# Kernel optimization log

Hardware: AMD Instinct MI355X
Metric: run time of the kernel (lower is better)

Reference implementation:

```python
import jax, jax.numpy as jnp
import numpy as np
import math

B, S, E, H, L = 16, 512, 256, 4, 2
D = E // H            # head size = 64
MAX_POS = 10
NUM_ITEMS = 50000


def setup_inputs() -> dict:
    key = jax.random.key(0)
    ks = jax.random.split(key, 16)
    s = 0.02
    item_inputs = jax.random.randint(ks[0], (B, S), 0, 2 * NUM_ITEMS + 1)
    item_ids = jax.random.randint(ks[1], (B, S), 0, NUM_ITEMS)
    input_embed = jax.random.normal(ks[2], (2 * NUM_ITEMS + 1, E), jnp.float32) * s
    input_embed = input_embed.at[0].set(0.0)  # padding_idx=0
    query_embed = jax.random.normal(ks[3], (NUM_ITEMS, E), jnp.float32) * s
    pos_key = jax.random.normal(ks[4], (MAX_POS, D), jnp.float32) * s
    pos_value = jax.random.normal(ks[5], (MAX_POS, D), jnp.float32) * s
    Wq = jax.random.normal(ks[6], (L, E, E), jnp.float32) * s
    bq = jnp.zeros((L, E), jnp.float32)
    Wk = jax.random.normal(ks[7], (L, E, E), jnp.float32) * s
    bk = jnp.zeros((L, E), jnp.float32)
    Wv = jax.random.normal(ks[8], (L, E, E), jnp.float32) * s
    bv = jnp.zeros((L, E), jnp.float32)
    Wo = jax.random.normal(ks[9], (L, E, E), jnp.float32) * s
    bo = jnp.zeros((L, E), jnp.float32)
    out_w = jax.random.normal(ks[10], (E, 1), jnp.float32) * s
    out_b = jnp.zeros((1,), jnp.float32)
    return dict(item_inputs=item_inputs, item_ids=item_ids,
                input_embed=input_embed, query_embed=query_embed,
                pos_key=pos_key, pos_value=pos_value,
                Wq=Wq, bq=bq, Wk=Wk, bk=bk, Wv=Wv, bv=bv, Wo=Wo, bo=bo,
                out_w=out_w, out_b=out_b)


def _heads(x, W, b):
    # [B,S,E] @ [E,E] -> [B,H,S,D]
    return (x @ W + b).reshape(B, S, H, D).transpose(0, 2, 1, 3)


def reference(item_inputs, item_ids, input_embed, query_embed, pos_key,
              pos_value, Wq, bq, Wk, bk, Wv, bv, Wo, bo, out_w, out_b):
    x = input_embed[item_inputs]          # [B,S,E]
    q_base = query_embed[item_ids]        # [B,S,E]

    i = jnp.arange(S)
    rel = jnp.clip(i[:, None] - i[None, :], 0, MAX_POS - 1)  # [S,S]
    pk = pos_key[rel]                     # [S,S,D]
    pv = pos_value[rel]                   # [S,S,D]
    causal = i[None, :] > i[:, None]      # future mask [S,S], True = masked
    scale = 1.0 / math.sqrt(D)

    out = x
    for l in range(L):
        qh = _heads(q_base, Wq[l], bq[l])
        kh = _heads(out, Wk[l], bk[l])
        vh = _heads(out, Wv[l], bv[l])
        # relative attention: scores = q.k^T + q.pos_key(i-j)
        scores = jnp.einsum('bhid,bhjd->bhij', qh, kh)
        scores = scores + jnp.einsum('bhid,ijd->bhij', qh, pk)
        scores = scores * scale
        scores = jnp.where(causal[None, None], -1e9, scores)
        p = jax.nn.softmax(scores, axis=-1)  # [B,H,S,S]
        # out_i = sum_j p_ij * (v_j + pos_value(i-j))
        attn = jnp.einsum('bhij,bhjd->bhid', p, vh) \
             + jnp.einsum('bhij,ijd->bhid', p, pv)
        merged = attn.transpose(0, 2, 1, 3).reshape(B, S, E)
        residual = merged @ Wo[l] + bo[l]
        out = out + jax.nn.relu(residual)
    return out @ out_w + out_b            # [B,S,1]
```

## Files before the change

### kernel.cpp

```cpp
#include <hip/hip_runtime.h>
#include <hip/hip_bf16.h>

#define B_ 16
#define S_ 512
#define E_ 256
#define H_ 4
#define D_ 64
#define L_ 2
#define MAXPOS 10
#define HS_ ((size_t)B_ * S_ * E_)

typedef __attribute__((ext_vector_type(8))) short bf16x8;
typedef __attribute__((ext_vector_type(4))) float f32x4;

static __device__ __forceinline__ short f2bf(float f) {
    __hip_bfloat16 h = __float2bfloat16(f);
    return __builtin_bit_cast(short, h);
}

static __device__ __forceinline__ void gload16(const void* g, void* l) {
    __builtin_amdgcn_global_load_lds(
        (const __attribute__((address_space(1))) void*)(g),
        (__attribute__((address_space(3))) void*)(l),
        16, 0, 0);
}

static __device__ __forceinline__ void stage_tile(const char* gbase, char* lds,
                                                  int w, int lane) {
    #pragma unroll
    for (int c = 0; c < 8; ++c) {
        const int L = (w * 8 + c) * 1024 + lane * 16;
        const int src = L ^ (((L >> 9) & 7) << 4);
        gload16(gbase + src, lds + (w * 8 + c) * 1024);
    }
}

static __device__ __forceinline__ void gemm4(const short* As, const short* Bs,
                                             int w, int l15, int l4,
                                             f32x4& a0, f32x4& a1,
                                             f32x4& a2, f32x4& a3) {
    const int sw = (l15 & 7) << 4;
    const int arow = w * 16 + l15;
    const f32x4 z4 = (f32x4){0.f, 0.f, 0.f, 0.f};
    a0 = z4; a1 = z4; a2 = z4; a3 = z4;
    #pragma unroll
    for (int ks = 0; ks < 8; ++ks) {
        const int coff = (ks * 64 + l4 * 16) ^ sw;
        const bf16x8 af = *reinterpret_cast<const bf16x8*>((const char*)As + arow * 512 + coff);
        const bf16x8 b0 = *reinterpret_cast<const bf16x8*>((const char*)Bs + (0 * 16 + l15) * 512 + coff);
        a0 = __builtin_amdgcn_mfma_f32_16x16x32_bf16(af, b0, a0, 0, 0, 0);
        const bf16x8 b1 = *reinterpret_cast<const bf16x8*>((const char*)Bs + (1 * 16 + l15) * 512 + coff);
        a1 = __builtin_amdgcn_mfma_f32_16x16x32_bf16(af, b1, a1, 0, 0, 0);
        const bf16x8 b2 = *reinterpret_cast<const bf16x8*>((const char*)Bs + (2 * 16 + l15) * 512 + coff);
        a2 = __builtin_amdgcn_mfma_f32_16x16x32_bf16(af, b2, a2, 0, 0, 0);
        const bf16x8 b3 = *reinterpret_cast<const bf16x8*>((const char*)Bs + (3 * 16 + l15) * 512 + coff);
        a3 = __builtin_amdgcn_mfma_f32_16x16x32_bf16(af, b3, a3, 0, 0, 0);
    }
}

static __device__ __forceinline__ void gemm_compute(const short* As, const short* Bs,
                                                    f32x4* acc, int w, int l15, int l4) {
    gemm4(As, Bs, w, l15, l4, acc[0], acc[1], acc[2], acc[3]);
}

__global__ __launch_bounds__(256) void setup_kernel(
    const int* __restrict__ item_inputs, const int* __restrict__ item_ids,
    const float* __restrict__ input_embed, const float* __restrict__ query_embed,
    const float* __restrict__ Wq, const float* __restrict__ Wk,
    const float* __restrict__ Wv, const float* __restrict__ Wo,
    const float* __restrict__ out_b,
    short* __restrict__ outb, short* __restrict__ qbb,
    short* __restrict__ Wt, float* __restrict__ y)
{
    const int tid = threadIdx.x;
    const int bx = blockIdx.x;
    if (bx < 512) {
        const int rr = tid >> 4, c0 = (tid & 15) * 16;
        const int row = bx * 16 + rr;
        const int ii = item_inputs[row];
        const int qi = item_ids[row];
        const float* xs = input_embed + (size_t)ii * E_ + c0;
        const float* qs = query_embed + (size_t)qi * E_ + c0;
        short* ob = outb + (size_t)row * E_ + c0;
        short* qb = qbb + (size_t)row * E_ + c0;
        #pragma unroll
        for (int q = 0; q < 4; ++q) {
            const float4 xv = reinterpret_cast<const float4*>(xs)[q];
            const float4 qv = reinterpret_cast<const float4*>(qs)[q];
            short4 xb = { f2bf(xv.x), f2bf(xv.y), f2bf(xv.z), f2bf(xv.w) };
            short4 qb4 = { f2bf(qv.x), f2bf(qv.y), f2bf(qv.z), f2bf(qv.w) };
            reinterpret_cast<short4*>(ob)[q] = xb;
            reinterpret_cast<short4*>(qb)[q] = qb4;
        }
        return;
    }
    const int pb = bx - 512;
    if (pb < 128) {
        __shared__ short tt[64 * 72];
        const int mId = pb >> 4;
        const int l = mId >> 2, which = mId & 3;
        const float* src = (which == 0 ? Wq : which == 1 ? Wk : which == 2 ? Wv : Wo)
                         + (size_t)l * E_ * E_;
        const int tr = (pb >> 2) & 3;
        const int tc = pb & 3;
        {
            const int kl = tid >> 2;
            const int nq = (tid & 3) * 16;
            const float* sp = src + (size_t)(tr * 64 + kl) * E_ + tc * 64 + nq;
            #pragma unroll
            for (int q = 0; q < 4; ++q) {
                const float4 v = reinterpret_cast<const float4*>(sp)[q];
                tt[(nq + q * 4 + 0) * 72 + kl] = f2bf(v.x);
                tt[(nq + q * 4 + 1) * 72 + kl] = f2bf(v.y);
                tt[(nq + q * 4 + 2) * 72 + kl] = f2bf(v.z);
                tt[(nq + q * 4 + 3) * 72 + kl] = f2bf(v.w);
            }
        }
        __syncthreads();
        {
            const int nl = tid >> 2;
            const int kq = (tid & 3) * 16;
            short* dst = Wt + (size_t)mId * 65536 + (size_t)(tc * 64 + nl) * E_ + tr * 64 + kq;
            *reinterpret_cast<bf16x8*>(&dst[0]) = *reinterpret_cast<const bf16x8*>(&tt[nl * 72 + kq]);
            *reinterpret_cast<bf16x8*>(&dst[8]) = *reinterpret_cast<const bf16x8*>(&tt[nl * 72 + kq + 8]);
        }
    } else if (pb == 128) {
        const float yb = out_b[0];
        for (int i = tid; i < 8192; i += 256) y[i] = yb;
    }
}

__global__ __launch_bounds__(256) void qkv0_kernel(
    const short* __restrict__ qbb, const short* __restrict__ outb,
    const short* __restrict__ Wt, const float* __restrict__ bq,
    const float* __restrict__ bk, const float* __restrict__ bv,
    const float* __restrict__ bq1, short* __restrict__ Qb,
    short* __restrict__ Qb1)
{
    __shared__ __align__(16) short As[64 * 256];
    __shared__ __align__(16) short Bs[64 * 256];
    const int bid = blockIdx.x;
    const int logical = (bid & 7) * 192 + (bid >> 3);
    const int bm = logical / 12;
    const int r = logical % 12;
    const int bn = r / 3, zp = r % 3;
    const int tid = threadIdx.x;
    const int lane = tid & 63, w = tid >> 6;
    const int l15 = lane & 15, l4 = lane >> 4;

    const short* A = (zp == 0) ? qbb : outb;
    const short* W0 = Wt + (size_t)zp * 65536;
    const float* bias0 = (zp == 0) ? bq : (zp == 1) ? bk : bv;
    short* C0 = Qb + (size_t)zp * HS_;

    stage_tile((const char*)A + (size_t)bm * 32768, (char*)As, w, lane);
    stage_tile((const char*)W0 + (size_t)bn * 32768, (char*)Bs, w, lane);
    __syncthreads();

    f32x4 acc[4];
    gemm_compute(As, Bs, acc, w, l15, l4);

    #pragma unroll
    for (int nf = 0; nf < 4; ++nf) {
        const int col = bn * 64 + nf * 16 + l15;
        const float bb = bias0[col];
        #pragma unroll
        for (int reg = 0; reg < 4; ++reg) {
            const int rowg = bm * 64 + w * 16 + l4 * 4 + reg;
            C0[(size_t)rowg * E_ + col] = f2bf(acc[nf][reg] + bb);
        }
    }

    if (zp == 0) {
        __syncthreads();
        stage_tile((const char*)(Wt + (size_t)4 * 65536) + (size_t)bn * 32768,
                   (char*)Bs, w, lane);
        __syncthreads();
        gemm_compute(As, Bs, acc, w, l15, l4);
        #pragma unroll
        for (int nf = 0; nf < 4; ++nf) {
            const int col = bn * 64 + nf * 16 + l15;
            const float bb = bq1[col];
            #pragma unroll
            for (int reg = 0; reg < 4; ++reg) {
                const int rowg = bm * 64 + w * 16 + l4 * 4 + reg;
                Qb1[(size_t)rowg * E_ + col] = f2bf(acc[nf][reg] + bb);
            }
        }
    }
}

__global__ __launch_bounds__(256) void kv1_kernel(
    const short* __restrict__ outb, const short* __restrict__ Wt1,
    const float* __restrict__ bk1, const float* __restrict__ bv1,
    short* __restrict__ Qb)
{
    __shared__ __align__(16) short As[64 * 256];
    __shared__ __align__(16) short Bs[64 * 256];
    const int bid = blockIdx.x;
    const int logical = (bid & 7) * 128 + (bid >> 3);
    const int bm = logical >> 3;
    const int r = logical & 7;
    const int bn = r >> 1, z = r & 1;
    const int tid = threadIdx.x;
    const int lane = tid & 63, w = tid >> 6;
    const int l15 = lane & 15, l4 = lane >> 4;

    const short* W = Wt1 + (size_t)(z + 1) * 65536;
    const float* bias = (z == 0) ? bk1 : bv1;

    stage_tile((const char*)outb + (size_t)bm * 32768, (char*)As, w, lane);
    stage_tile((const char*)W + (size_t)bn * 32768, (char*)Bs, w, lane);
    __syncthreads();

    f32x4 acc[4];
    gemm_compute(As, Bs, acc, w, l15, l4);

    short* Cz = Qb + (size_t)(z + 1) * HS_;
    #pragma unroll
    for (int nf = 0; nf < 4; ++nf) {
        const int col = bn * 64 + nf * 16 + l15;
        const float bb = bias[col];
        #pragma unroll
        for (int reg = 0; reg < 4; ++reg) {
            const int rowg = bm * 64 + w * 16 + l4 * 4 + reg;
            Cz[(size_t)rowg * E_ + col] = f2bf(acc[nf][reg] + bb);
        }
    }
}

__global__ __launch_bounds__(256) void o0_kernel(
    const short* __restrict__ mgb, const short* __restrict__ Wo_t,
    const float* __restrict__ bo0, const int* __restrict__ item_inputs,
    const float* __restrict__ input_embed, float* __restrict__ outf,
    short* __restrict__ outb)
{
    __shared__ __align__(16) short As[64 * 256];
    __shared__ __align__(16) short Bs[64 * 256];
    const int bid = blockIdx.x;
    const int logical = (bid & 7) * 64 + (bid >> 3);
    const int bm = logical >> 2, bn = logical & 3;
    const int tid = threadIdx.x;
    const int lane = tid & 63, w = tid >> 6;
    const int l15 = lane & 15, l4 = lane >> 4;

    stage_tile((const char*)mgb + (size_t)bm * 32768, (char*)As, w, lane);
    stage_tile((const char*)Wo_t + (size_t)bn * 32768, (char*)Bs, w, lane);
    __syncthreads();

    f32x4 acc[4];
    gemm_compute(As, Bs, acc, w, l15, l4);

    #pragma unroll
    for (int reg = 0; reg < 4; ++reg) {
        const int rowg = bm * 64 + w * 16 + l4 * 4 + reg;
        const int ii = item_inputs[rowg];
        const float* emb = input_embed + (size_t)ii * E_;
        #pragma unroll
        for (int nf = 0; nf < 4; ++nf) {
            const int col = bn * 64 + nf * 16 + l15;
            const size_t idx = (size_t)rowg * E_ + col;
            const float o = emb[col] + fmaxf(acc[nf][reg] + bo0[col], 0.0f);
            outf[idx] = o;
            outb[idx] = f2bf(o);
        }
    }
}

__global__ __launch_bounds__(256) void attn_kernel(
    const short* __restrict__ Q, const short* __restrict__ K,
    const short* __restrict__ V, const float* __restrict__ pos_key,
    const float* __restrict__ pos_value, short* __restrict__ merged)
{
    __shared__ __align__(16) short Qs[64 * 72];
    __shared__ __align__(16) short Ks[2][64 * 64];
    __shared__ __align__(16) short Vts[2][4656];
    __shared__ __align__(16) short Pl[4 * 16 * 72];
    __shared__ __align__(16) short Pk[16 * 72];
    __shared__ float pv_sh[MAXPOS * 64];
    __shared__ float qpk_sh[64 * 16];
    __shared__ float pdiag[64 * 9];

    const int bid = blockIdx.x;
    const int half = bid >> 8;
    const int g = bid & 255;
    const int tp = g & 3;
    const int bh = g >> 2;
    const int it = half ? tp : 7 - tp;
    const int h = bh & 3;
    const int b = bh >> 2;
    const int tid = threadIdx.x;
    const int lane = tid & 63;
    const int w = tid >> 6;
    const int l15 = lane & 15;
    const int l4  = lane >> 4;
    const int rloc  = l4 * 4;
    const int rbase = w * 16 + rloc;
    const int swl = (l15 & 7) << 4;
    const float SC = 0.18033688f;

    const size_t boff = (size_t)(b * S_) * E_ + h * D_;

    const int vrow = tid >> 2, vdq = (tid & 3) * 16;
    const int vskew = (tid & 3) * 32 + vrow * 2;
    auto issueK = [&](int jt, int buf) {
        const char* Kb = (const char*)(K + boff + (size_t)(jt * 64) * E_);
        #pragma unroll
        for (int c = 0; c < 2; ++c) {
            const int chunk = w * 2 + c;
            const int row = chunk * 8 + (lane >> 3);
            const int col = (lane & 7) * 16;
            const int src = row * 512 + (col ^ ((row & 7) << 4));
            gload16(Kb + src, (char*)Ks[buf] + chunk * 1024);
        }
    };
    auto issueV = [&](int jt, bf16x8& v0, bf16x8& v1) {
        const short* vp = &V[boff + (size_t)(jt * 64 + vrow) * E_ + vdq];
        v0 = *reinterpret_cast<const bf16x8*>(vp);
        v1 = *reinterpret_cast<const bf16x8*>(vp + 8);
    };
    auto writeV = [&](int buf, const bf16x8& v0, const bf16x8& v1) {
        #pragma unroll
        for (int e = 0; e < 8; ++e) {
            *(short*)((char*)Vts[buf] + (vdq + e) * 144 + vskew) = v0[e];
            *(short*)((char*)Vts[buf] + (vdq + 8 + e) * 144 + vskew) = v1[e];
        }
    };

    issueK(0, 0);
    bf16x8 vc0, vc1;
    issueV(0, vc0, vc1);

    for (int idx = tid; idx < MAXPOS * 64; idx += 256) pv_sh[idx] = pos_value[idx];
    for (int idx = tid; idx < 64 * 9; idx += 256) pdiag[idx] = 0.0f;
    for (int idx = tid; idx < 16 * 64; idx += 256) {
        const int r = idx >> 6, d = idx & 63;
        Pk[r * 72 + d] = (r < MAXPOS) ? f2bf(pos_key[r * 64 + d]) : (short)0;
    }
    {
        const int row = tid >> 2, dq = (tid & 3) * 16;
        const short* qp = &Q[boff + (size_t)(it * 64 + row) * E_ + dq];
        *reinterpret_cast<bf16x8*>(&Qs[row * 72 + dq]) = *reinterpret_cast<const bf16x8*>(qp);
        *reinterpret_cast<bf16x8*>(&Qs[row * 72 + dq + 8]) = *reinterpret_cast<const bf16x8*>(qp + 8);
    }
    writeV(0, vc0, vc1);
    __syncthreads();

    bf16x8 aq[2];
    #pragma unroll
    for (int ks = 0; ks < 2; ++ks)
        aq[ks] = *reinterpret_cast<const bf16x8*>(&Qs[(w * 16 + l15) * 72 + ks * 32 + 8 * l4]);

    f32x4 cq = (f32x4){0.f, 0.f, 0.f, 0.f};
    #pragma unroll
    for (int ks = 0; ks < 2; ++ks) {
        const bf16x8 bpk = *reinterpret_cast<const bf16x8*>(&Pk[l15 * 72 + ks * 32 + 8 * l4]);
        cq = __builtin_amdgcn_mfma_f32_16x16x32_bf16(aq[ks], bpk, cq, 0, 0, 0);
    }
    float q9[4];
    #pragma unroll
    for (int r = 0; r < 4; ++r) {
        qpk_sh[(rbase + r) * 16 + l15] = cq[r] * SC;
        q9[r] = __shfl(cq[r], l4 * 16 + 9, 64) * SC;
    }

    f32x4 accv[4];
    #pragma unroll
    for (int nf = 0; nf < 4; ++nf) accv[nf] = (f32x4){0.f, 0.f, 0.f, 0.f};
    float ls[4] = {0.f, 0.f, 0.f, 0.f};

    for (int jt = 0; jt <= it; ++jt) {
        const int cur = jt & 1;
        bf16x8 vn0, vn1;
        if (jt < it) {
            issueK(jt + 1, cur ^ 1);
            issueV(jt + 1, vn0, vn1);
        }

        f32x4 cs[4];
        __builtin_amdgcn_s_setprio(1);
        #pragma unroll
        for (int nf = 0; nf < 4; ++nf) {
            const int jrow = nf * 16 + l15;
            const bf16x8 bk0 = *reinterpret_cast<const bf16x8*>(
                (const char*)Ks[cur] + jrow * 128 + ((l4 * 16) ^ swl));
            const bf16x8 bk1 = *reinterpret_cast<const bf16x8*>(
                (const char*)Ks[cur] + jrow * 128 + ((64 + l4 * 16) ^ swl));
            f32x4 c = (f32x4){0.f, 0.f, 0.f, 0.f};
            c = __builtin_amdgcn_mfma_f32_16x16x32_bf16(aq[0], bk0, c, 0, 0, 0);
            cs[nf] = __builtin_amdgcn_mfma_f32_16x16x32_bf16(aq[1], bk1, c, 0, 0, 0);
        }
        __builtin_amdgcn_s_setprio(0);

        const bool near = (jt >= it - 1);
        #pragma unroll
        for (int nf = 0; nf < 4; ++nf) {
            const int j = jt * 64 + nf * 16 + l15;
            #pragma unroll
            for (int r = 0; r < 4; ++r) {
                float pp;
                if (near) {
                    const int i = it * 64 + rbase + r;
                    const int rel = i - j;
                    if (rel < 0) pp = 0.0f;
                    else {
                        const int rc = rel < 9 ? rel : 9;
                        pp = exp2f(fmaf(cs[nf][r], SC, qpk_sh[(rbase + r) * 16 + rc]));
                        if (rel < 9) pdiag[(rbase + r) * 9 + rel] = pp;
                    }
                } else {
                    pp = exp2f(fmaf(cs[nf][r], SC, q9[r]));
                }
                ls[r] += pp;
                Pl[w * 1152 + (rloc + r) * 72 + nf * 16 + l15] = f2bf(pp);
            }
        }

        __builtin_amdgcn_s_setprio(1);
        #pragma unroll
        for (int ks = 0; ks < 2; ++ks) {
            const bf16x8 pa = *reinterpret_cast<const bf16x8*>(
                &Pl[w * 1152 + l15 * 72 + ks * 32 + 8 * l4]);
            #pragma unroll
            for (int nf = 0; nf < 4; ++nf) {
                const int d = nf * 16 + l15;
                const bf16x8 bv = *reinterpret_cast<const bf16x8*>(
                    (const char*)Vts[cur] + d * 144 + nf * 32 + ks * 64 + l4 * 16);
                accv[nf] = __builtin_amdgcn_mfma_f32_16x16x32_bf16(pa, bv, accv[nf], 0, 0, 0);
            }
        }
        __builtin_amdgcn_s_setprio(0);

        if (jt < it) {
            writeV(cur ^ 1, vn0, vn1);
            __syncthreads();
        }
    }

    #pragma unroll
    for (int m = 1; m < 16; m <<= 1) {
        #pragma unroll
        for (int r = 0; r < 4; ++r) ls[r] += __shfl_xor(ls[r], m, 64);
    }

    #pragma unroll
    for (int r = 0; r < 4; ++r) {
        const int rowl = rbase + r;
        const float inv = 1.0f / ls[r];
        #pragma unroll
        for (int nf = 0; nf < 4; ++nf) {
            const int col = nf * 16 + l15;
            const float pv9 = pv_sh[9 * 64 + col];
            float extra = ls[r] * pv9;
            #pragma unroll
            for (int rr = 0; rr < 9; ++rr)
                extra += pdiag[rowl * 9 + rr] * (pv_sh[rr * 64 + col] - pv9);
            merged[boff + (size_t)(it * 64 + rowl) * E_ + col] =
                f2bf((accv[nf][r] + extra) * inv);
        }
    }
}

__global__ __launch_bounds__(256) void o1final_kernel(
    const short* __restrict__ mgb, const short* __restrict__ Wt7,
    const float* __restrict__ bo1, const float* __restrict__ outf,
    const float* __restrict__ fw, float* __restrict__ y)
{
    __shared__ __align__(16) short As[64 * 256];
    __shared__ __align__(16) short Bs[64 * 256];
    const int bid = blockIdx.x;
    const int logical = (bid & 7) * 64 + (bid >> 3);
    const int bm = logical >> 2, bn = logical & 3;
    const int tid = threadIdx.x;
    const int lane = tid & 63, w = tid >> 6;
    const int l15 = lane & 15, l4 = lane >> 4;

    stage_tile((const char*)mgb + (size_t)bm * 32768, (char*)As, w, lane);
    stage_tile((const char*)Wt7 + (size_t)bn * 32768, (char*)Bs, w, lane);
    __syncthreads();

    f32x4 acc[4];
    gemm_compute(As, Bs, acc, w, l15, l4);

    float s[4] = {0.f, 0.f, 0.f, 0.f};
    #pragma unroll
    for (int nf = 0; nf < 4; ++nf) {
        const int col = bn * 64 + nf * 16 + l15;
        const float bb = bo1[col];
        const float fwv = fw[col];
        #pragma unroll
        for (int reg = 0; reg < 4; ++reg) {
            const int rowg = bm * 64 + w * 16 + l4 * 4 + reg;
            const float o = outf[(size_t)rowg * E_ + col] + fmaxf(acc[nf][reg] + bb, 0.0f);
            s[reg] += o * fwv;
        }
    }
    #pragma unroll
    for (int m = 1; m < 16; m <<= 1) {
        #pragma unroll
        for (int reg = 0; reg < 4; ++reg) s[reg] += __shfl_xor(s[reg], m, 64);
    }
    if (l15 == 0) {
        #pragma unroll
        for (int reg = 0; reg < 4; ++reg)
            atomicAdd(&y[bm * 64 + w * 16 + l4 * 4 + reg], s[reg]);
    }
}

extern "C" void kernel_launch(void* const* d_in, const int* in_sizes, int n_in,
                              void* d_out, int out_size, void* d_ws, size_t ws_size,
                              hipStream_t stream) {
    const int*   item_inputs = (const int*)d_in[0];
    const int*   item_ids    = (const int*)d_in[1];
    const float* input_embed = (const float*)d_in[2];
    const float* query_embed = (const float*)d_in[3];
    const float* pos_key     = (const float*)d_in[4];
    const float* pos_value   = (const float*)d_in[5];
    const float* Wq = (const float*)d_in[6];
    const float* bq = (const float*)d_in[7];
    const float* Wk = (const float*)d_in[8];
    const float* bk = (const float*)d_in[9];
    const float* Wv = (const float*)d_in[10];
    const float* bv = (const float*)d_in[11];
    const float* Wo = (const float*)d_in[12];
    const float* bo = (const float*)d_in[13];
    const float* out_w = (const float*)d_in[14];
    const float* out_b = (const float*)d_in[15];
    float* y = (float*)d_out;

    char* w8 = (char*)d_ws;
    float* outf = (float*)(w8);
    short* outb = (short*)(w8 + ((size_t)8  << 20));
    short* qbb  = (short*)(w8 + ((size_t)12 << 20));
    short* Qb   = (short*)(w8 + ((size_t)16 << 20));
    short* mgb  = (short*)(w8 + ((size_t)28 << 20));
    short* Wt   = (short*)(w8 + ((size_t)32 << 20));
    short* Qb1  = (short*)(w8 + ((size_t)34 << 20));

    setup_kernel<<<641, 256, 0, stream>>>(
        item_inputs, item_ids, input_embed, query_embed,
        Wq, Wk, Wv, Wo, out_b, outb, qbb, Wt, y);

    qkv0_kernel<<<1536, 256, 0, stream>>>(
        qbb, outb, Wt, bq, bk, bv, bq + E_, Qb, Qb1);
    attn_kernel<<<512, 256, 0, stream>>>(
        Qb, Qb + HS_, Qb + 2 * HS_, pos_key, pos_value, mgb);
    o0_kernel<<<512, 256, 0, stream>>>(
        mgb, Wt + (size_t)3 * 65536, bo, item_inputs, input_embed, outf, outb);

    kv1_kernel<<<1024, 256, 0, stream>>>(
        outb, Wt + (size_t)4 * 65536, bk + E_, bv + E_, Qb);
    attn_kernel<<<512, 256, 0, stream>>>(
        Qb1, Qb + HS_, Qb + 2 * HS_, pos_key, pos_value, mgb);
    o1final_kernel<<<512, 256, 0, stream>>>(
        mgb, Wt + (size_t)7 * 65536, bo + E_, outf, out_w, y);
}
```

Baseline: 91.76 us.

## Fuse embedding gather and weight transpose into the layer-0 QKV GEMM kernel

Removes the separate setup kernel. The layer-0 QKV GEMM blocks now gather embedding rows, convert them to bf16 and write them straight into swizzled LDS. They also read the fp32 Wq/Wk/Wv directly, transposing them into LDS instead of staging pre-converted bf16 tiles. Extra blocks in the same launch transpose only the weights later kernels need (Wo0, Wk1, Wv1, Wo1) and initialise y. This saves a launch and the bf16 intermediate round trip. In exchange, every GEMM block redundantly converts fp32 weights and embeddings, using scalar 2-byte LDS stores, which may be costly.

```diff
diff --git a/kernel.cpp b/kernel.cpp
--- a/kernel.cpp
+++ b/kernel.cpp
@@ -63,103 +63,113 @@
     gemm4(As, Bs, w, l15, l4, acc[0], acc[1], acc[2], acc[3]);
 }
 
-__global__ __launch_bounds__(256) void setup_kernel(
+__global__ __launch_bounds__(256) void qkv0g_kernel(
     const int* __restrict__ item_inputs, const int* __restrict__ item_ids,
     const float* __restrict__ input_embed, const float* __restrict__ query_embed,
     const float* __restrict__ Wq, const float* __restrict__ Wk,
     const float* __restrict__ Wv, const float* __restrict__ Wo,
+    const float* __restrict__ bq, const float* __restrict__ bk,
+    const float* __restrict__ bv, const float* __restrict__ bq1,
     const float* __restrict__ out_b,
-    short* __restrict__ outb, short* __restrict__ qbb,
+    short* __restrict__ Qb, short* __restrict__ Qb1,
     short* __restrict__ Wt, float* __restrict__ y)
-{
-    const int tid = threadIdx.x;
-    const int bx = blockIdx.x;
-    if (bx < 512) {
-        const int rr = tid >> 4, c0 = (tid & 15) * 16;
-        const int row = bx * 16 + rr;
-        const int ii = item_inputs[row];
-        const int qi = item_ids[row];
-        const float* xs = input_embed + (size_t)ii * E_ + c0;
-        const float* qs = query_embed + (size_t)qi * E_ + c0;
-        short* ob = outb + (size_t)row * E_ + c0;
-        short* qb = qbb + (size_t)row * E_ + c0;
-        #pragma unroll
-        for (int q = 0; q < 4; ++q) {
-            const float4 xv = reinterpret_cast<const float4*>(xs)[q];
-            const float4 qv = reinterpret_cast<const float4*>(qs)[q];
-            short4 xb = { f2bf(xv.x), f2bf(xv.y), f2bf(xv.z), f2bf(xv.w) };
-            short4 qb4 = { f2bf(qv.x), f2bf(qv.y), f2bf(qv.z), f2bf(qv.w) };
-            reinterpret_cast<short4*>(ob)[q] = xb;
-            reinterpret_cast<short4*>(qb)[q] = qb4;
-        }
-        return;
-    }
-    const int pb = bx - 512;
-    if (pb < 128) {
-        __shared__ short tt[64 * 72];
-        const int mId = pb >> 4;
-        const int l = mId >> 2, which = mId & 3;
-        const float* src = (which == 0 ? Wq : which == 1 ? Wk : which == 2 ? Wv : Wo)
-                         + (size_t)l * E_ * E_;
-        const int tr = (pb >> 2) & 3;
-        const int tc = pb & 3;
-        {
-            const int kl = tid >> 2;
-            const int nq = (tid & 3) * 16;
-            const float* sp = src + (size_t)(tr * 64 + kl) * E_ + tc * 64 + nq;
-            #pragma unroll
-            for (int q = 0; q < 4; ++q) {
-                const float4 v = reinterpret_cast<const float4*>(sp)[q];
-                tt[(nq + q * 4 + 0) * 72 + kl] = f2bf(v.x);
-                tt[(nq + q * 4 + 1) * 72 + kl] = f2bf(v.y);
-                tt[(nq + q * 4 + 2) * 72 + kl] = f2bf(v.z);
-                tt[(nq + q * 4 + 3) * 72 + kl] = f2bf(v.w);
-            }
-        }
-        __syncthreads();
-        {
-            const int nl = tid >> 2;
-            const int kq = (tid & 3) * 16;
-            short* dst = Wt + (size_t)mId * 65536 + (size_t)(tc * 64 + nl) * E_ + tr * 64 + kq;
-            *reinterpret_cast<bf16x8*>(&dst[0]) = *reinterpret_cast<const bf16x8*>(&tt[nl * 72 + kq]);
-            *reinterpret_cast<bf16x8*>(&dst[8]) = *reinterpret_cast<const bf16x8*>(&tt[nl * 72 + kq + 8]);
-        }
-    } else if (pb == 128) {
-        const float yb = out_b[0];
-        for (int i = tid; i < 8192; i += 256) y[i] = yb;
-    }
-}
-
-__global__ __launch_bounds__(256) void qkv0_kernel(
-    const short* __restrict__ qbb, const short* __restrict__ outb,
-    const short* __restrict__ Wt, const float* __restrict__ bq,
-    const float* __restrict__ bk, const float* __restrict__ bv,
-    const float* __restrict__ bq1, short* __restrict__ Qb,
-    short* __restrict__ Qb1)
 {
     __shared__ __align__(16) short As[64 * 256];
     __shared__ __align__(16) short Bs[64 * 256];
     const int bid = blockIdx.x;
-    const int logical = (bid & 7) * 192 + (bid >> 3);
-    const int bm = logical / 12;
-    const int r = logical % 12;
+    const int tid = threadIdx.x;
+
+    if (bid >= 1536) {
+        const int pb = bid - 1536;
+        if (pb < 64) {
+            short* tt = As;
+            const int m = pb >> 4;
+            const int slot = (m == 0) ? 3 : (m == 1) ? 5 : (m == 2) ? 6 : 7;
+            const float* src = (m == 0) ? Wo : (m == 1) ? (Wk + 65536)
+                             : (m == 2) ? (Wv + 65536) : (Wo + 65536);
+            const int tpb = pb & 15;
+            const int tr = tpb >> 2, tc = tpb & 3;
+            {
+                const int kl = tid >> 2;
+                const int nq = (tid & 3) * 16;
+                const float* sp = src + (size_t)(tr * 64 + kl) * E_ + tc * 64 + nq;
+                #pragma unroll
+                for (int q = 0; q < 4; ++q) {
+                    const float4 v = reinterpret_cast<const float4*>(sp)[q];
+                    tt[(nq + q * 4 + 0) * 72 + kl] = f2bf(v.x);
+                    tt[(nq + q * 4 + 1) * 72 + kl] = f2bf(v.y);
+                    tt[(nq + q * 4 + 2) * 72 + kl] = f2bf(v.z);
+                    tt[(nq + q * 4 + 3) * 72 + kl] = f2bf(v.w);
+                }
+            }
+            __syncthreads();
+            {
+                const int nl = tid >> 2;
+                const int kq = (tid & 3) * 16;
+                short* dst = Wt + (size_t)slot * 65536 + (size_t)(tc * 64 + nl) * E_ + tr * 64 + kq;
+                *reinterpret_cast<bf16x8*>(&dst[0]) = *reinterpret_cast<const bf16x8*>(&tt[nl * 72 + kq]);
+                *reinterpret_cast<bf16x8*>(&dst[8]) = *reinterpret_cast<const bf16x8*>(&tt[nl * 72 + kq + 8]);
+            }
+        } else {
+            const float yb = out_b[0];
+            for (int i = tid; i < 8192; i += 256) y[i] = yb;
+        }
+        return;
+    }
+
+    const int bm = bid / 12;
+    const int r = bid % 12;
     const int bn = r / 3, zp = r % 3;
-    const int tid = threadIdx.x;
     const int lane = tid & 63, w = tid >> 6;
     const int l15 = lane & 15, l4 = lane >> 4;
 
-    const short* A = (zp == 0) ? qbb : outb;
-    const short* W0 = Wt + (size_t)zp * 65536;
+    {
+        const int rl = tid >> 2;
+        const int row = bm * 64 + rl;
+        const int gi = (zp == 0) ? item_ids[row] : item_inputs[row];
+        const float* src = ((zp == 0) ? query_embed : input_embed)
+                         + (size_t)gi * E_ + (tid & 3) * 64;
+        const int cb = (tid & 3) * 128;
+        const int s = (rl & 7) << 4;
+        #pragma unroll
+        for (int j = 0; j < 8; ++j) {
+            const float4 v0 = reinterpret_cast<const float4*>(src)[j * 2];
+            const float4 v1 = reinterpret_cast<const float4*>(src)[j * 2 + 1];
+            bf16x8 t;
+            t[0] = f2bf(v0.x); t[1] = f2bf(v0.y); t[2] = f2bf(v0.z); t[3] = f2bf(v0.w);
+            t[4] = f2bf(v1.x); t[5] = f2bf(v1.y); t[6] = f2bf(v1.z); t[7] = f2bf(v1.w);
+            *reinterpret_cast<bf16x8*>((char*)As + rl * 512 + ((cb + j * 16) ^ s)) = t;
+        }
+    }
+
+    auto transposeW = [&](const float* W0) {
+        #pragma unroll
+        for (int p = 0; p < 4; ++p) {
+            const int kl = tid >> 2;
+            const int k = p * 64 + kl;
+            const int nq = (tid & 3) * 16;
+            const float* sp = W0 + (size_t)k * E_ + bn * 64 + nq;
+            #pragma unroll
+            for (int q = 0; q < 4; ++q) {
+                const float4 v = reinterpret_cast<const float4*>(sp)[q];
+                const int n0 = nq + q * 4;
+                *(short*)((char*)Bs + (n0 + 0) * 512 + ((2 * k) ^ (((n0 + 0) & 7) << 4))) = f2bf(v.x);
+                *(short*)((char*)Bs + (n0 + 1) * 512 + ((2 * k) ^ (((n0 + 1) & 7) << 4))) = f2bf(v.y);
+                *(short*)((char*)Bs + (n0 + 2) * 512 + ((2 * k) ^ (((n0 + 2) & 7) << 4))) = f2bf(v.z);
+                *(short*)((char*)Bs + (n0 + 3) * 512 + ((2 * k) ^ (((n0 + 3) & 7) << 4))) = f2bf(v.w);
+            }
+        }
+    };
+
+    const float* W0 = (zp == 0) ? Wq : (zp == 1) ? Wk : Wv;
+    transposeW(W0);
+    __syncthreads();
+
+    f32x4 acc[4];
+    gemm_compute(As, Bs, acc, w, l15, l4);
+
     const float* bias0 = (zp == 0) ? bq : (zp == 1) ? bk : bv;
     short* C0 = Qb + (size_t)zp * HS_;
-
-    stage_tile((const char*)A + (size_t)bm * 32768, (char*)As, w, lane);
-    stage_tile((const char*)W0 + (size_t)bn * 32768, (char*)Bs, w, lane);
-    __syncthreads();
-
-    f32x4 acc[4];
-    gemm_compute(As, Bs, acc, w, l15, l4);
-
     #pragma unroll
     for (int nf = 0; nf < 4; ++nf) {
         const int col = bn * 64 + nf * 16 + l15;
@@ -173,8 +183,7 @@
 
     if (zp == 0) {
         __syncthreads();
-        stage_tile((const char*)(Wt + (size_t)4 * 65536) + (size_t)bn * 32768,
-                   (char*)Bs, w, lane);
+        transposeW(Wq + 65536);
         __syncthreads();
         gemm_compute(As, Bs, acc, w, l15, l4);
         #pragma unroll
@@ -531,27 +540,27 @@
     char* w8 = (char*)d_ws;
     float* outf = (float*)(w8);
     short* outb = (short*)(w8 + ((size_t)8  << 20));
-    short* qbb  = (short*)(w8 + ((size_t)12 << 20));
     short* Qb   = (short*)(w8 + ((size_t)16 << 20));
     short* mgb  = (short*)(w8 + ((size_t)28 << 20));
     short* Wt   = (short*)(w8 + ((size_t)32 << 20));
     short* Qb1  = (short*)(w8 + ((size_t)34 << 20));
 
-    setup_kernel<<<641, 256, 0, stream>>>(
+    qkv0g_kernel<<<1601, 256, 0, stream>>>(
         item_inputs, item_ids, input_embed, query_embed,
-        Wq, Wk, Wv, Wo, out_b, outb, qbb, Wt, y);
-
-    qkv0_kernel<<<1536, 256, 0, stream>>>(
-        qbb, outb, Wt, bq, bk, bv, bq + E_, Qb, Qb1);
+        Wq, Wk, Wv, Wo, bq, bk, bv, bq + E_, out_b, Qb, Qb1, Wt, y);
+
     attn_kernel<<<512, 256, 0, stream>>>(
         Qb, Qb + HS_, Qb + 2 * HS_, pos_key, pos_value, mgb);
+
     o0_kernel<<<512, 256, 0, stream>>>(
         mgb, Wt + (size_t)3 * 65536, bo, item_inputs, input_embed, outf, outb);
 
     kv1_kernel<<<1024, 256, 0, stream>>>(
         outb, Wt + (size_t)4 * 65536, bk + E_, bv + E_, Qb);
+
     attn_kernel<<<512, 256, 0, stream>>>(
         Qb1, Qb + HS_, Qb + 2 * HS_, pos_key, pos_value, mgb);
+
     o1final_kernel<<<512, 256, 0, stream>>>(
         mgb, Wt + (size_t)7 * 65536, bo + E_, outf, out_w, y);
 }
```

Result: slower. 105.2 us (+14.6%).
